# Optimization experiments

Hardware: AMD Instinct MI355X
Metric: run time of the kernel (lower is better)

## Reference

```python
import jax, jax.numpy as jnp
import numpy as np

N, K, IN, FEAT, H, OUT, E = 30000, 25, 64, 32, 128, 64, 480000


def setup_inputs() -> dict:
    key = jax.random.key(0)
    ks = jax.random.split(key, 24)
    w = lambda k, shp: (jax.random.normal(k, shp, dtype=jnp.float32) * 0.05)
    z = lambda n: jnp.zeros((n,), jnp.float32)
    return {
        "x": jax.random.normal(ks[0], (N, IN), jnp.float32),
        "dists_max": jax.random.uniform(ks[1], (N, K), jnp.float32),
        "dists_argmax": jax.random.randint(ks[2], (N, K), 0, N, jnp.int32),
        "edge_index": jax.random.randint(ks[3], (2, E), 0, N, jnp.int32),
        "train_mask": jnp.ones((E,), jnp.int32),
        # PGNN.linear_pre: in -> 32
        "w_pre": w(ks[4], (IN, FEAT)), "b_pre": z(FEAT),
        # conv_first (PGNN_layer(32, 128))
        "l1_dc_w1": w(ks[5], (1, H)), "l1_dc_b1": z(H),
        "l1_dc_w2": w(ks[6], (H, 1)), "l1_dc_b2": z(1),
        "l1_wh": w(ks[7], (2 * FEAT, H)), "l1_bh": z(H),
        "l1_wp": w(ks[8], (H, 1)), "l1_bp": z(1),
        # conv_out (PGNN_layer(128, 128))
        "l2_dc_w1": w(ks[9], (1, H)), "l2_dc_b1": z(H),
        "l2_dc_w2": w(ks[10], (H, 1)), "l2_dc_b2": z(1),
        "l2_wh": w(ks[11], (2 * H, H)), "l2_bh": z(H),
        "l2_wp": w(ks[12], (H, 1)), "l2_bp": z(1),
        # GNNModel.layers[1]: Linear(len_distmax=25 -> hidden=128)
        "w_lin": w(ks[13], (K, H)), "b_lin": z(H),
        # FeedForwardNetwork(2H -> 2H -> OUT)
        "ff_w1": w(ks[14], (2 * H, 2 * H)), "ff_b1": z(2 * H),
        "ff_w2": w(ks[15], (2 * H, OUT)), "ff_b2": z(OUT),
    }


def _nonlinear(d, w1, b1, w2, b2):
    # Nonlinear(1, H, 1) applied to dists: [N, K] -> [N, K]
    h = jax.nn.relu(d[..., None] @ w1 + b1)  # [N, K, H]
    return (h @ w2 + b2)[..., 0]


def _pgnn_layer(feat, dmax, argmax, dc_w1, dc_b1, dc_w2, dc_b2, wh, bh, wp, bp):
    d = _nonlinear(dmax, dc_w1, dc_b1, dc_w2, dc_b2)          # [N, K]
    sub = feat[argmax]                                         # gather: [N, K, F]
    self_feat = jnp.broadcast_to(feat[:, None, :], sub.shape)  # [N, K, F]
    msgs = jnp.concatenate([sub * d[..., None], self_feat], axis=-1)  # [N, K, 2F]
    msgs = jax.nn.relu(msgs @ wh + bh)                         # [N, K, H]
    out_position = (msgs @ wp + bp)[..., 0]                    # [N, K]
    out_structure = msgs.mean(axis=1)                          # [N, H]
    return out_position, out_structure


def reference(x, dists_max, dists_argmax, edge_index, train_mask,
              w_pre, b_pre,
              l1_dc_w1, l1_dc_b1, l1_dc_w2, l1_dc_b2, l1_wh, l1_bh, l1_wp, l1_bp,
              l2_dc_w1, l2_dc_b1, l2_dc_w2, l2_dc_b2, l2_wh, l2_bh, l2_wp, l2_bp,
              w_lin, b_lin, ff_w1, ff_b1, ff_w2, ff_b2):
    # PGNN (layer_num=2, feature_pre=True)
    h = x @ w_pre + b_pre                                      # [N, 32]
    _, h = _pgnn_layer(h, dists_max, dists_argmax,
                       l1_dc_w1, l1_dc_b1, l1_dc_w2, l1_dc_b2,
                       l1_wh, l1_bh, l1_wp, l1_bp)             # [N, H]
    x_pos, _ = _pgnn_layer(h, dists_max, dists_argmax,
                           l2_dc_w1, l2_dc_b1, l2_dc_w2, l2_dc_b2,
                           l2_wh, l2_bh, l2_wp, l2_bp)         # [N, K]
    # F.normalize(p=2, dim=-1) with eps=1e-12
    norm = jnp.maximum(jnp.linalg.norm(x_pos, axis=-1, keepdims=True), 1e-12)
    h = jax.nn.relu(x_pos / norm)                              # act after layer 0
    h = jax.nn.relu(h @ w_lin + b_lin)                         # layers[1] + act, [N, H]
    # get_minibatch_embeddings: select train edges, gather endpoint embeddings
    idx = np.where(np.asarray(train_mask) == 1)[0]
    ei = edge_index[:, idx]
    e = jnp.concatenate([h[ei[0]], h[ei[1]]], axis=1)          # [E_train, 2H]
    # FeedForwardNetwork
    e = jax.nn.relu(e @ ff_w1 + ff_b1)
    return e @ ff_w2 + ff_b2                                   # [E_train, OUT]
```

## Files before the change

kernel.cpp:

```cpp
#include <hip/hip_runtime.h>
#include <hip/hip_bf16.h>
#include <cmath>

#define NN 30000
#define KK 25
#define IN_F 64
#define FEAT 32
#define HH 128
#define OUTF 64
#define EE 480000
#define NPAGE 469
#define NB (8 * NPAGE)
#define LUTN 4096

typedef __attribute__((ext_vector_type(8))) _Float16 fp16x8;
typedef __attribute__((ext_vector_type(2))) _Float16 h2v;
typedef __attribute__((ext_vector_type(16))) float f32x16;

__device__ inline float u2f(unsigned u) { return __builtin_bit_cast(float, u); }
__device__ inline unsigned short f2b(float f) {
    __bf16 h = (__bf16)f;
    return __builtin_bit_cast(unsigned short, h);
}
__device__ inline unsigned short f2h(float f) {
    _Float16 h = (_Float16)f;
    return __builtin_bit_cast(unsigned short, h);
}
__device__ inline float blo(unsigned u) { return u2f(u << 16); }
__device__ inline float bhi(unsigned u) { return u2f(u & 0xffff0000u); }

__device__ inline unsigned hrelu2(unsigned a, unsigned b) {
    h2v x = __builtin_bit_cast(h2v, a);
    h2v y = __builtin_bit_cast(h2v, b);
    h2v s = x + y;
    h2v z = {(_Float16)0.f, (_Float16)0.f};
    h2v r = __builtin_elementwise_max(s, z);
    return __builtin_bit_cast(unsigned, r);
}

__device__ inline float lut_eval(const float* __restrict__ lut, float dm) {
    float tt = dm * (float)LUTN;
    int i0 = (int)tt;
    i0 = i0 < 0 ? 0 : (i0 > LUTN - 1 ? LUTN - 1 : i0);
    float f = tt - (float)i0;
    float l0 = lut[i0];
    return fmaf(lut[i0 + 1] - l0, f, l0);
}

__global__ void k_prep(const float* __restrict__ x,
                       const float* __restrict__ w_pre, const float* __restrict__ b_pre,
                       const float* __restrict__ l1wh, const float* __restrict__ l1bh,
                       const float* __restrict__ ffw2, const float* __restrict__ ffw1,
                       const float* __restrict__ l2wh,
                       const float* __restrict__ l1w1, const float* __restrict__ l1b1,
                       const float* __restrict__ l1w2, const float* __restrict__ l1b2,
                       const float* __restrict__ l2w1, const float* __restrict__ l2b1,
                       const float* __restrict__ l2w2, const float* __restrict__ l2b2,
                       unsigned* __restrict__ hist,
                       float* __restrict__ lut1, float* __restrict__ lut2,
                       unsigned short* __restrict__ xh, unsigned short* __restrict__ xl,
                       float* __restrict__ bfuse, unsigned short* __restrict__ wt,
                       unsigned short* __restrict__ wt1,
                       unsigned short* __restrict__ wt2h, unsigned short* __restrict__ wt2l,
                       unsigned short* __restrict__ wfh, unsigned short* __restrict__ wfl) {
    int gid = blockIdx.x * 256 + threadIdx.x;
    if (gid < NB) { hist[gid] = 0u; return; }
    gid -= NB;
    if (gid < 2 * (LUTN + 1)) {
        int which = gid / (LUTN + 1);
        int i = gid % (LUTN + 1);
        float dm = (float)i * (1.0f / (float)LUTN);
        const float* w1 = which ? l2w1 : l1w1;
        const float* b1 = which ? l2b1 : l1b1;
        const float* w2 = which ? l2w2 : l1w2;
        const float* b2 = which ? l2b2 : l1b2;
        float a = 0.f;
        for (int h = 0; h < HH; ++h)
            a = fmaf(fmaxf(fmaf(dm, w1[h], b1[h]), 0.f), w2[h], a);
        (which ? lut2 : lut1)[i] = a + b2[0];
        return;
    }
    gid -= 2 * (LUTN + 1);
    if (gid < NN * IN_F / 8) {
        int i = gid * 8;
        unsigned short vh[8], vl[8];
#pragma unroll
        for (int j = 0; j < 8; ++j) {
            float v = x[i + j];
            _Float16 hi = (_Float16)v;
            vh[j] = __builtin_bit_cast(unsigned short, hi);
            vl[j] = f2h((v - (float)hi) * 1024.f);
        }
        *(uint4*)(xh + i) = *(uint4*)vh;
        *(uint4*)(xl + i) = *(uint4*)vl;
        return;
    }
    gid -= NN * IN_F / 8;
    if (gid < 256) {
        int half = gid >> 7, h = gid & 127;
        const float* wh = l1wh + half * FEAT * HH + h;
        float acc = (half == 1) ? l1bh[h] : 0.f;
#pragma unroll
        for (int c = 0; c < FEAT; ++c) acc = fmaf(b_pre[c], wh[c * HH], acc);
        bfuse[gid] = acc;
    } else if (gid < 16640) {
        int i = gid - 256;
        int k = i >> 6, c = i & 63;
        wt[c * 256 + k] = f2h(ffw2[i]);
    } else if (gid < 82176) {
        int i = gid - 16640;
        int c = i >> 7, j = i & 127;
        float v = (c < 256) ? ffw1[j * 256 + c] : ffw1[(128 + j) * 256 + (c - 256)];
        wt1[c * 128 + j] = f2h(v);
    } else if (gid < 114944) {
        int i = gid - 82176;
        int c = i >> 7, j = i & 127;
        float v = (c < 128) ? l2wh[j * 128 + c] : l2wh[(128 + j) * 128 + (c - 128)];
        _Float16 hi = (_Float16)v;
        wt2h[c * 128 + j] = __builtin_bit_cast(unsigned short, hi);
        wt2l[c * 128 + j] = f2h((v - (float)hi) * 1024.f);
    } else if (gid < 131328) {
        int i = gid - 114944;
        int cc = i >> 6, j = i & 63;
        const float* wrow = w_pre + j * FEAT;
        float acc = 0.f;
#pragma unroll
        for (int c = 0; c < FEAT; ++c) {
            float wh = (cc < 128) ? l1wh[c * HH + cc] : l1wh[(FEAT + c) * HH + (cc - 128)];
            acc = fmaf(wrow[c], wh, acc);
        }
        _Float16 hi = (_Float16)acc;
        wfh[cc * 64 + j] = __builtin_bit_cast(unsigned short, hi);
        wfl[cc * 64 + j] = f2h((acc - (float)hi) * 1024.f);
    }
}

__global__ void k_hist(const int* __restrict__ ei, unsigned* __restrict__ hist) {
    int base = (blockIdx.x * 256 + threadIdx.x) * 8;
    if (base >= EE) return;
    int4 s0 = *(const int4*)(ei + base);
    int4 s1 = *(const int4*)(ei + base + 4);
    int4 d0 = *(const int4*)(ei + EE + base);
    int4 d1 = *(const int4*)(ei + EE + base + 4);
    int ss[8] = {s0.x, s0.y, s0.z, s0.w, s1.x, s1.y, s1.z, s1.w};
    int dd[8] = {d0.x, d0.y, d0.z, d0.w, d1.x, d1.y, d1.z, d1.w};
#pragma unroll
    for (int j = 0; j < 8; ++j) {
        int key = (ss[j] * 8 / NN) * NPAGE + (dd[j] >> 6);
        atomicAdd(&hist[key], 1u);
    }
}

__global__ __launch_bounds__(64) void k_scan(const unsigned* __restrict__ hist,
                                             unsigned* __restrict__ cursor) {
    int l = threadIdx.x;
    const int PER = 59;
    unsigned tot = 0;
    for (int j = 0; j < PER; ++j) {
        int i = l * PER + j;
        if (i < NB) tot += hist[i];
    }
    unsigned run = tot;
#pragma unroll
    for (int off = 1; off < 64; off <<= 1) {
        unsigned u = __shfl_up(run, off, 64);
        if (l >= off) run += u;
    }
    unsigned base = run - tot;
    for (int j = 0; j < PER; ++j) {
        int i = l * PER + j;
        if (i < NB) {
            cursor[i] = base;
            base += hist[i];
        }
    }
}

__global__ void k_scatter(const int* __restrict__ ei, unsigned* __restrict__ cursor,
                          uint4* __restrict__ sedge) {
    int base = (blockIdx.x * 256 + threadIdx.x) * 8;
    if (base >= EE) return;
    int4 s0 = *(const int4*)(ei + base);
    int4 s1 = *(const int4*)(ei + base + 4);
    int4 d0 = *(const int4*)(ei + EE + base);
    int4 d1 = *(const int4*)(ei + EE + base + 4);
    int ss[8] = {s0.x, s0.y, s0.z, s0.w, s1.x, s1.y, s1.z, s1.w};
    int dd[8] = {d0.x, d0.y, d0.z, d0.w, d1.x, d1.y, d1.z, d1.w};
    unsigned pp[8];
#pragma unroll
    for (int j = 0; j < 8; ++j) {
        int key = (ss[j] * 8 / NN) * NPAGE + (dd[j] >> 6);
        pp[j] = atomicAdd(&cursor[key], 1u);
    }
#pragma unroll
    for (int j = 0; j < 8; ++j)
        sedge[pp[j]] = make_uint4((unsigned)ss[j], (unsigned)dd[j], (unsigned)(base + j), 0u);
}

template <int KD>
__global__ __launch_bounds__(256) void k_nodegemm(
    const unsigned short* __restrict__ Ah, const unsigned short* __restrict__ Al,
    const unsigned short* __restrict__ Wh, const unsigned short* __restrict__ Wl,
    const float* __restrict__ gbias, const float* __restrict__ sbias,
    unsigned short* __restrict__ Gb, float* __restrict__ S) {
    int t = threadIdx.x;
    int l = t & 63, w = t >> 6;
    int c = l & 31, kh = l >> 5;
    int nb = blockIdx.x * 32;
    int na = nb + c;
    if (na >= NN) na = NN - 1;
    fp16x8 afh[KD / 16], afl[KD / 16];
#pragma unroll
    for (int kt = 0; kt < KD / 16; ++kt) {
        afh[kt] = *(const fp16x8*)(Ah + na * KD + kt * 16 + kh * 8);
        afl[kt] = *(const fp16x8*)(Al + na * KD + kt * 16 + kh * 8);
    }
    f32x16 acch0, acch1, accl0, accl1;
#pragma unroll
    for (int i = 0; i < 16; ++i) { acch0[i] = 0.f; acch1[i] = 0.f; accl0[i] = 0.f; accl1[i] = 0.f; }
    int cb0 = w * 64, cb1 = w * 64 + 32;
#pragma unroll
    for (int kt = 0; kt < KD / 16; ++kt) {
        fp16x8 b0h = *(const fp16x8*)(Wh + (cb0 + c) * KD + kt * 16 + kh * 8);
        fp16x8 b0l = *(const fp16x8*)(Wl + (cb0 + c) * KD + kt * 16 + kh * 8);
        fp16x8 b1h = *(const fp16x8*)(Wh + (cb1 + c) * KD + kt * 16 + kh * 8);
        fp16x8 b1l = *(const fp16x8*)(Wl + (cb1 + c) * KD + kt * 16 + kh * 8);
        acch0 = __builtin_amdgcn_mfma_f32_32x32x16_f16(afh[kt], b0h, acch0, 0, 0, 0);
        accl0 = __builtin_amdgcn_mfma_f32_32x32x16_f16(afh[kt], b0l, accl0, 0, 0, 0);
        accl0 = __builtin_amdgcn_mfma_f32_32x32x16_f16(afl[kt], b0h, accl0, 0, 0, 0);
        acch1 = __builtin_amdgcn_mfma_f32_32x32x16_f16(afh[kt], b1h, acch1, 0, 0, 0);
        accl1 = __builtin_amdgcn_mfma_f32_32x32x16_f16(afh[kt], b1l, accl1, 0, 0, 0);
        accl1 = __builtin_amdgcn_mfma_f32_32x32x16_f16(afl[kt], b1h, accl1, 0, 0, 0);
    }
    const float inv1024 = 1.0f / 1024.0f;
#pragma unroll
    for (int half = 0; half < 2; ++half) {
        int col = (half ? cb1 : cb0) + c;
        bool isG = col < HH;
        float gb_ = (isG && gbias) ? gbias[col] : 0.f;
        float sb_ = (!isG) ? sbias[col - HH] : 0.f;
#pragma unroll
        for (int r = 0; r < 16; ++r) {
            int row = (r & 3) + 8 * (r >> 2) + 4 * kh;
            int n = nb + row;
            float v = half ? (acch1[r] + accl1[r] * inv1024)
                           : (acch0[r] + accl0[r] * inv1024);
            if (n < NN) {
                if (isG) Gb[n * HH + col] = f2b(v + gb_);
                else S[n * HH + (col - HH)] = v + sb_;
            }
        }
    }
}

__global__ void k_layer1(const unsigned* __restrict__ G1u, const float* __restrict__ S1,
                         const float* __restrict__ dmax, const float* __restrict__ lut1,
                         const int* __restrict__ amax,
                         unsigned* __restrict__ hh, unsigned* __restrict__ hl) {
    int t = threadIdx.x;
    int n = blockIdx.x * 4 + (t >> 6);
    int l = t & 63;
    float2 sv = *(const float2*)(S1 + n * HH + 2 * l);
    const int* arow = amax + n * KK;
    const float* drow = dmax + n * KK;
    float dk[KK];
#pragma unroll
    for (int k = 0; k < KK; ++k) dk[k] = lut_eval(lut1, drow[k]);
    float acc0 = 0.f, acc1 = 0.f;
#pragma unroll
    for (int k = 0; k < KK; ++k) {
        int a = arow[k];
        unsigned g = G1u[a * 64 + l];
        acc0 += fmaxf(fmaf(dk[k], blo(g), sv.x), 0.f);
        acc1 += fmaxf(fmaf(dk[k], bhi(g), sv.y), 0.f);
    }
    float a0 = acc0 * 0.04f, a1 = acc1 * 0.04f;
    _Float16 h0 = (_Float16)a0, h1v = (_Float16)a1;
    float r0 = (a0 - (float)h0) * 1024.f, r1 = (a1 - (float)h1v) * 1024.f;
    hh[n * 64 + l] = (unsigned)__builtin_bit_cast(unsigned short, h0) |
                     ((unsigned)__builtin_bit_cast(unsigned short, h1v) << 16);
    hl[n * 64 + l] = (unsigned)f2h(r0) | ((unsigned)f2h(r1) << 16);
}

__global__ __launch_bounds__(256) void k_xpos2(
    const unsigned* __restrict__ G2u, const float* __restrict__ S2,
    const float* __restrict__ dmax, const float* __restrict__ lut2,
    const int* __restrict__ amax,
    const float* __restrict__ wp, const float* __restrict__ bp,
    const float* __restrict__ wlin, const float* __restrict__ blin,
    unsigned short* __restrict__ hl16) {
    __shared__ float xs[28];
    int t = threadIdx.x;
    int n = blockIdx.x;
    int w = t >> 6, l = t & 63;
    float2 sv = *(const float2*)(S2 + n * HH + 2 * l);
    float2 wpv = *(const float2*)(wp + 2 * l);
    float bpv = bp[0];
    const int* arow = amax + n * KK;
    const float* drow = dmax + n * KK;
    int kcnt = (w == 0) ? 7 : 6;
    unsigned gv[7];
    float dk[7];
#pragma unroll
    for (int j = 0; j < 7; ++j) {
        if (j < kcnt) {
            int k = w + 4 * j;
            gv[j] = G2u[arow[k] * 64 + l];
        }
    }
#pragma unroll
    for (int j = 0; j < 7; ++j) {
        if (j < kcnt) dk[j] = lut_eval(lut2, drow[w + 4 * j]);
    }
    float v[7];
#pragma unroll
    for (int j = 0; j < 7; ++j) {
        if (j < kcnt) {
            v[j] = fmaxf(fmaf(dk[j], blo(gv[j]), sv.x), 0.f) * wpv.x +
                   fmaxf(fmaf(dk[j], bhi(gv[j]), sv.y), 0.f) * wpv.y;
        }
    }
#pragma unroll
    for (int s = 1; s < 64; s <<= 1) {
#pragma unroll
        for (int j = 0; j < 7; ++j) {
            if (j < kcnt) v[j] += __shfl_xor(v[j], s, 64);
        }
    }
    if (l == 0) {
#pragma unroll
        for (int j = 0; j < 7; ++j) {
            if (j < kcnt) xs[w + 4 * j] = v[j] + bpv;
        }
    }
    __syncthreads();
    if (t < HH) {
        float ss = 0.f;
#pragma unroll
        for (int k = 0; k < KK; ++k) { float xv = xs[k]; ss = fmaf(xv, xv, ss); }
        float inv = 1.0f / fmaxf(sqrtf(ss), 1e-12f);
        float acc = blin[t];
#pragma unroll
        for (int k = 0; k < KK; ++k) {
            float xv = fmaxf(xs[k], 0.f) * inv;
            acc = fmaf(xv, wlin[k * HH + t], acc);
        }
        hl16[n * HH + t] = f2h(fmaxf(acc, 0.f));
    }
}

__global__ __launch_bounds__(256) void k_ab_mfma(
    const unsigned short* __restrict__ hl16, const unsigned short* __restrict__ wt1,
    const float* __restrict__ ffb1, unsigned short* __restrict__ ab) {
    int t = threadIdx.x;
    int l = t & 63, w = t >> 6;
    int c = l & 31, kh = l >> 5;
    int nb = blockIdx.x * 32;
    int na = nb + c;
    if (na >= NN) na = NN - 1;
    fp16x8 af[8];
#pragma unroll
    for (int kt = 0; kt < 8; ++kt)
        af[kt] = *(const fp16x8*)(hl16 + na * 128 + kt * 16 + kh * 8);
    f32x16 acc[4];
#pragma unroll
    for (int g = 0; g < 4; ++g)
#pragma unroll
        for (int i = 0; i < 16; ++i) acc[g][i] = 0.f;
#pragma unroll
    for (int kt = 0; kt < 8; ++kt) {
#pragma unroll
        for (int g = 0; g < 4; ++g) {
            fp16x8 b = *(const fp16x8*)(wt1 + (w * 128 + g * 32 + c) * 128 + kt * 16 + kh * 8);
            acc[g] = __builtin_amdgcn_mfma_f32_32x32x16_f16(af[kt], b, acc[g], 0, 0, 0);
        }
    }
#pragma unroll
    for (int g = 0; g < 4; ++g) {
        int col = w * 128 + g * 32 + c;
        float bias = (col >= 256) ? ffb1[col - 256] : 0.f;
#pragma unroll
        for (int r = 0; r < 16; ++r) {
            int row = (r & 3) + 8 * (r >> 2) + 4 * kh;
            int n = nb + row;
            if (n < NN) ab[n * 512 + col] = f2h(acc[g][r] + bias);
        }
    }
}

__global__ __launch_bounds__(256, 2) void k_edge_mfma(
    const unsigned short* __restrict__ abf, const uint4* __restrict__ sedge,
    const unsigned short* __restrict__ wt, const float* __restrict__ ffb2,
    float* __restrict__ out) {
    __shared__ uint4 P[4][32 * 32];
    int t = threadIdx.x;
    int l = t & 63;
    int w = t >> 6;
    int c = l & 31, kh = l >> 5;
    uint4* Pw = P[w];

    fp16x8 wf0[16], wf1[16];
#pragma unroll
    for (int kt = 0; kt < 16; ++kt) {
        wf0[kt] = *(const fp16x8*)(wt + c * 256 + kt * 16 + kh * 8);
        wf1[kt] = *(const fp16x8*)(wt + (c + 32) * 256 + kt * 16 + kh * 8);
    }
    float bias0 = ffb2[c], bias1 = ffb2[c + 32];

    int xcd = blockIdx.x & 7;
    int slot = blockIdx.x >> 3;
    int seg = c;
    int rh = l >> 5;

    for (int tl = slot; tl < NPAGE; tl += 64) {
        int tbw = (xcd * NPAGE + tl) * 128 + w * 32;
#pragma unroll 4
        for (int it = 0; it < 16; ++it) {
            int row = it * 2 + rh;
            int pos = tbw + row;
            uint4 rec = sedge[pos < EE ? pos : EE - 1];
            uint4 a = *(const uint4*)(abf + (size_t)rec.x * 512 + seg * 8);
            uint4 b = *(const uint4*)(abf + (size_t)rec.y * 512 + 256 + seg * 8);
            uint4 p;
            p.x = hrelu2(a.x, b.x);
            p.y = hrelu2(a.y, b.y);
            p.z = hrelu2(a.z, b.z);
            p.w = hrelu2(a.w, b.w);
            Pw[row * 32 + (seg ^ (row & 15))] = p;
        }
        asm volatile("s_waitcnt lgkmcnt(0)" ::: "memory");
        __builtin_amdgcn_sched_barrier(0);
        f32x16 acc0, acc1;
#pragma unroll
        for (int i = 0; i < 16; ++i) { acc0[i] = 0.f; acc1[i] = 0.f; }
#pragma unroll
        for (int kt = 0; kt < 16; ++kt) {
            int idx = (kt * 2 + kh) ^ (c & 15);
            fp16x8 af = __builtin_bit_cast(fp16x8, Pw[c * 32 + idx]);
            acc0 = __builtin_amdgcn_mfma_f32_32x32x16_f16(af, wf0[kt], acc0, 0, 0, 0);
            acc1 = __builtin_amdgcn_mfma_f32_32x32x16_f16(af, wf1[kt], acc1, 0, 0, 0);
        }
        int spos = tbw + c;
        int eid = (int)sedge[spos < EE ? spos : EE - 1].z;
        int rbase = 4 * kh;
#pragma unroll
        for (int r = 0; r < 16; ++r) {
            int row = (r & 3) + 8 * (r >> 2) + rbase;
            int eidr = __shfl(eid, row, 64);
            if (tbw + row < EE) {
                size_t o = (size_t)eidr * 64;
                out[o + c] = acc0[r] + bias0;
                out[o + 32 + c] = acc1[r] + bias1;
            }
        }
        __builtin_amdgcn_sched_barrier(0);
    }
}

extern "C" void kernel_launch(void* const* d_in, const int* in_sizes, int n_in,
                              void* d_out, int out_size, void* d_ws, size_t ws_size,
                              hipStream_t stream) {
    const float* x     = (const float*)d_in[0];
    const float* dmax  = (const float*)d_in[1];
    const int*   amax  = (const int*)d_in[2];
    const int*   ei    = (const int*)d_in[3];
    const float* w_pre = (const float*)d_in[5];
    const float* b_pre = (const float*)d_in[6];
    const float* l1w1  = (const float*)d_in[7];
    const float* l1b1  = (const float*)d_in[8];
    const float* l1w2  = (const float*)d_in[9];
    const float* l1b2  = (const float*)d_in[10];
    const float* l1wh  = (const float*)d_in[11];
    const float* l1bh  = (const float*)d_in[12];
    const float* l2w1  = (const float*)d_in[15];
    const float* l2b1  = (const float*)d_in[16];
    const float* l2w2  = (const float*)d_in[17];
    const float* l2b2  = (const float*)d_in[18];
    const float* l2wh  = (const float*)d_in[19];
    const float* l2bh  = (const float*)d_in[20];
    const float* l2wp  = (const float*)d_in[21];
    const float* l2bp  = (const float*)d_in[22];
    const float* wlin  = (const float*)d_in[23];
    const float* blin  = (const float*)d_in[24];
    const float* ffw1  = (const float*)d_in[25];
    const float* ffb1  = (const float*)d_in[26];
    const float* ffw2  = (const float*)d_in[27];
    const float* ffb2  = (const float*)d_in[28];

    float* ws = (float*)d_ws;
    unsigned short* Gb = (unsigned short*)(ws + 1500000);
    float* S  = ws + 3500000;
    unsigned short* xh = (unsigned short*)(ws + 7500000);
    unsigned short* xl = (unsigned short*)(ws + 8500000);
    unsigned* hhp = (unsigned*)(ws + 9500000);
    unsigned* hlp = (unsigned*)(ws + 11500000);
    unsigned short* hl16 = (unsigned short*)(ws + 13500000);
    uint4* sedge = (uint4*)(ws + 15500000);
    unsigned short* wfh = (unsigned short*)(ws + 17500000);
    unsigned short* wfl = (unsigned short*)(ws + 17510000);
    float* bfuse = ws + 17520000;
    unsigned short* wt = (unsigned short*)(ws + 17530000);
    unsigned short* wt1 = (unsigned short*)(ws + 17540000);
    unsigned short* wt2h = (unsigned short*)(ws + 17580000);
    unsigned short* wt2l = (unsigned short*)(ws + 17600000);
    unsigned* hist = (unsigned*)(ws + 17620000);
    unsigned* cursor = (unsigned*)(ws + 17630000);
    float* lut1 = ws + 17640000;
    float* lut2 = ws + 17645000;
    unsigned short* ab = (unsigned short*)ws;
    float* out = (float*)d_out;

    k_prep<<<1498, 256, 0, stream>>>(x, w_pre, b_pre, l1wh, l1bh, ffw2, ffw1, l2wh,
                                     l1w1, l1b1, l1w2, l1b2, l2w1, l2b1, l2w2, l2b2,
                                     hist, lut1, lut2, xh, xl,
                                     bfuse, wt, wt1, wt2h, wt2l, wfh, wfl);
    k_hist<<<(EE / 8 + 255) / 256, 256, 0, stream>>>(ei, hist);
    k_scan<<<1, 64, 0, stream>>>(hist, cursor);
    k_scatter<<<(EE / 8 + 255) / 256, 256, 0, stream>>>(ei, cursor, sedge);

    k_nodegemm<IN_F><<<938, 256, 0, stream>>>(xh, xl, wfh, wfl, bfuse, bfuse + 128, Gb, S);
    k_layer1<<<NN / 4, 256, 0, stream>>>((const unsigned*)Gb, S, dmax, lut1, amax, hhp, hlp);
    k_nodegemm<HH><<<938, 256, 0, stream>>>((const unsigned short*)hhp,
                                            (const unsigned short*)hlp, wt2h, wt2l,
                                            nullptr, l2bh, Gb, S);
    k_xpos2<<<NN, 256, 0, stream>>>((const unsigned*)Gb, S, dmax, lut2, amax,
                                    l2wp, l2bp, wlin, blin, hl16);
    k_ab_mfma<<<938, 256, 0, stream>>>(hl16, wt1, ffb1, ab);

    k_edge_mfma<<<512, 256, 0, stream>>>(ab, sedge, wt, ffb2, out);
}
```

Measured before the change: 364.1 us.

## Restructure xpos2 to one node per wave and share edge tile block-wide

k_layer1 and k_xpos2 now issue all 25 gathers up front, ahead of the LUT evaluation, so more loads are in flight at once. k_xpos2 is remapped so each wave handles a whole node: it reduces all 25 positions with shuffles, does the normalize and the 25-to-128 linear layer in registers, and drops the shared-memory pass and block barrier. The grid shrinks fourfold. k_edge_mfma now builds one shared 128-row tile cooperatively with all 256 threads and uses __syncthreads instead of per-wave LDS regions, at the cost of block-level synchronisation and higher register pressure from the 25-entry arrays.

```diff
diff --git a/kernel.cpp b/kernel.cpp
--- a/kernel.cpp
+++ b/kernel.cpp
@@ -263,16 +263,18 @@
     float2 sv = *(const float2*)(S1 + n * HH + 2 * l);
     const int* arow = amax + n * KK;
     const float* drow = dmax + n * KK;
-    float dk[KK];
-#pragma unroll
-    for (int k = 0; k < KK; ++k) dk[k] = lut_eval(lut1, drow[k]);
+    unsigned gvv[KK];
+#pragma unroll
+    for (int k = 0; k < KK; ++k) gvv[k] = G1u[arow[k] * 64 + l];
+    float dm_[KK];
+#pragma unroll
+    for (int k = 0; k < KK; ++k) dm_[k] = drow[k];
     float acc0 = 0.f, acc1 = 0.f;
 #pragma unroll
     for (int k = 0; k < KK; ++k) {
-        int a = arow[k];
-        unsigned g = G1u[a * 64 + l];
-        acc0 += fmaxf(fmaf(dk[k], blo(g), sv.x), 0.f);
-        acc1 += fmaxf(fmaf(dk[k], bhi(g), sv.y), 0.f);
+        float dkv = lut_eval(lut1, dm_[k]);
+        acc0 += fmaxf(fmaf(dkv, blo(gvv[k]), sv.x), 0.f);
+        acc1 += fmaxf(fmaf(dkv, bhi(gvv[k]), sv.y), 0.f);
     }
     float a0 = acc0 * 0.04f, a1 = acc1 * 0.04f;
     _Float16 h0 = (_Float16)a0, h1v = (_Float16)a1;
@@ -288,65 +290,47 @@
     const int* __restrict__ amax,
     const float* __restrict__ wp, const float* __restrict__ bp,
     const float* __restrict__ wlin, const float* __restrict__ blin,
-    unsigned short* __restrict__ hl16) {
-    __shared__ float xs[28];
+    unsigned* __restrict__ hl16u) {
     int t = threadIdx.x;
-    int n = blockIdx.x;
     int w = t >> 6, l = t & 63;
+    int n = blockIdx.x * 4 + w;
     float2 sv = *(const float2*)(S2 + n * HH + 2 * l);
     float2 wpv = *(const float2*)(wp + 2 * l);
-    float bpv = bp[0];
     const int* arow = amax + n * KK;
     const float* drow = dmax + n * KK;
-    int kcnt = (w == 0) ? 7 : 6;
-    unsigned gv[7];
-    float dk[7];
-#pragma unroll
-    for (int j = 0; j < 7; ++j) {
-        if (j < kcnt) {
-            int k = w + 4 * j;
-            gv[j] = G2u[arow[k] * 64 + l];
-        }
-    }
-#pragma unroll
-    for (int j = 0; j < 7; ++j) {
-        if (j < kcnt) dk[j] = lut_eval(lut2, drow[w + 4 * j]);
-    }
-    float v[7];
-#pragma unroll
-    for (int j = 0; j < 7; ++j) {
-        if (j < kcnt) {
-            v[j] = fmaxf(fmaf(dk[j], blo(gv[j]), sv.x), 0.f) * wpv.x +
-                   fmaxf(fmaf(dk[j], bhi(gv[j]), sv.y), 0.f) * wpv.y;
-        }
+    unsigned gvv[KK];
+#pragma unroll
+    for (int k = 0; k < KK; ++k) gvv[k] = G2u[arow[k] * 64 + l];
+    float dm_[KK];
+#pragma unroll
+    for (int k = 0; k < KK; ++k) dm_[k] = drow[k];
+    float v[KK];
+#pragma unroll
+    for (int k = 0; k < KK; ++k) {
+        float dkv = lut_eval(lut2, dm_[k]);
+        v[k] = fmaxf(fmaf(dkv, blo(gvv[k]), sv.x), 0.f) * wpv.x +
+               fmaxf(fmaf(dkv, bhi(gvv[k]), sv.y), 0.f) * wpv.y;
     }
 #pragma unroll
     for (int s = 1; s < 64; s <<= 1) {
 #pragma unroll
-        for (int j = 0; j < 7; ++j) {
-            if (j < kcnt) v[j] += __shfl_xor(v[j], s, 64);
-        }
-    }
-    if (l == 0) {
-#pragma unroll
-        for (int j = 0; j < 7; ++j) {
-            if (j < kcnt) xs[w + 4 * j] = v[j] + bpv;
-        }
-    }
-    __syncthreads();
-    if (t < HH) {
-        float ss = 0.f;
-#pragma unroll
-        for (int k = 0; k < KK; ++k) { float xv = xs[k]; ss = fmaf(xv, xv, ss); }
-        float inv = 1.0f / fmaxf(sqrtf(ss), 1e-12f);
-        float acc = blin[t];
-#pragma unroll
-        for (int k = 0; k < KK; ++k) {
-            float xv = fmaxf(xs[k], 0.f) * inv;
-            acc = fmaf(xv, wlin[k * HH + t], acc);
-        }
-        hl16[n * HH + t] = f2h(fmaxf(acc, 0.f));
-    }
+        for (int k = 0; k < KK; ++k) v[k] += __shfl_xor(v[k], s, 64);
+    }
+    float bpv = bp[0];
+    float ss = 0.f;
+#pragma unroll
+    for (int k = 0; k < KK; ++k) { v[k] += bpv; ss = fmaf(v[k], v[k], ss); }
+    float inv = 1.0f / fmaxf(sqrtf(ss), 1e-12f);
+    float acc0 = blin[2 * l], acc1 = blin[2 * l + 1];
+#pragma unroll
+    for (int k = 0; k < KK; ++k) {
+        float xv = fmaxf(v[k], 0.f) * inv;
+        float2 wl = *(const float2*)(wlin + k * HH + 2 * l);
+        acc0 = fmaf(xv, wl.x, acc0);
+        acc1 = fmaf(xv, wl.y, acc1);
+    }
+    hl16u[n * 64 + l] = (unsigned)f2h(fmaxf(acc0, 0.f)) |
+                        ((unsigned)f2h(fmaxf(acc1, 0.f)) << 16);
 }
 
 __global__ __launch_bounds__(256) void k_ab_mfma(
@@ -392,12 +376,11 @@
     const unsigned short* __restrict__ abf, const uint4* __restrict__ sedge,
     const unsigned short* __restrict__ wt, const float* __restrict__ ffb2,
     float* __restrict__ out) {
-    __shared__ uint4 P[4][32 * 32];
+    __shared__ uint4 P[128 * 32];
     int t = threadIdx.x;
     int l = t & 63;
     int w = t >> 6;
     int c = l & 31, kh = l >> 5;
-    uint4* Pw = P[w];
 
     fp16x8 wf0[16], wf1[16];
 #pragma unroll
@@ -409,15 +392,15 @@
 
     int xcd = blockIdx.x & 7;
     int slot = blockIdx.x >> 3;
-    int seg = c;
-    int rh = l >> 5;
+    int seg = t & 31;
+    int rb = t >> 5;
 
     for (int tl = slot; tl < NPAGE; tl += 64) {
-        int tbw = (xcd * NPAGE + tl) * 128 + w * 32;
+        int tb = (xcd * NPAGE + tl) * 128;
 #pragma unroll 4
-        for (int it = 0; it < 16; ++it) {
-            int row = it * 2 + rh;
-            int pos = tbw + row;
+        for (int r = 0; r < 16; ++r) {
+            int row = r * 8 + rb;
+            int pos = tb + row;
             uint4 rec = sedge[pos < EE ? pos : EE - 1];
             uint4 a = *(const uint4*)(abf + (size_t)rec.x * 512 + seg * 8);
             uint4 b = *(const uint4*)(abf + (size_t)rec.y * 512 + 256 + seg * 8);
@@ -426,34 +409,36 @@
             p.y = hrelu2(a.y, b.y);
             p.z = hrelu2(a.z, b.z);
             p.w = hrelu2(a.w, b.w);
-            Pw[row * 32 + (seg ^ (row & 15))] = p;
-        }
-        asm volatile("s_waitcnt lgkmcnt(0)" ::: "memory");
-        __builtin_amdgcn_sched_barrier(0);
+            int col = (seg * 16) ^ ((row & 15) << 4);
+            P[row * 32 + (col >> 4)] = p;
+        }
+        __syncthreads();
         f32x16 acc0, acc1;
 #pragma unroll
         for (int i = 0; i < 16; ++i) { acc0[i] = 0.f; acc1[i] = 0.f; }
+        int wrow = w * 32 + c;
+        int sw = (wrow & 15) << 4;
 #pragma unroll
         for (int kt = 0; kt < 16; ++kt) {
-            int idx = (kt * 2 + kh) ^ (c & 15);
-            fp16x8 af = __builtin_bit_cast(fp16x8, Pw[c * 32 + idx]);
+            int col = (kt * 32 + kh * 16) ^ sw;
+            fp16x8 af = __builtin_bit_cast(fp16x8, P[wrow * 32 + (col >> 4)]);
             acc0 = __builtin_amdgcn_mfma_f32_32x32x16_f16(af, wf0[kt], acc0, 0, 0, 0);
             acc1 = __builtin_amdgcn_mfma_f32_32x32x16_f16(af, wf1[kt], acc1, 0, 0, 0);
         }
-        int spos = tbw + c;
+        int spos = tb + wrow;
         int eid = (int)sedge[spos < EE ? spos : EE - 1].z;
         int rbase = 4 * kh;
 #pragma unroll
         for (int r = 0; r < 16; ++r) {
             int row = (r & 3) + 8 * (r >> 2) + rbase;
             int eidr = __shfl(eid, row, 64);
-            if (tbw + row < EE) {
+            if (tb + w * 32 + row < EE) {
                 size_t o = (size_t)eidr * 64;
                 out[o + c] = acc0[r] + bias0;
                 out[o + 32 + c] = acc1[r] + bias1;
             }
         }
-        __builtin_amdgcn_sched_barrier(0);
+        __syncthreads();
     }
 }
 
@@ -523,8 +508,8 @@
     k_nodegemm<HH><<<938, 256, 0, stream>>>((const unsigned short*)hhp,
                                             (const unsigned short*)hlp, wt2h, wt2l,
                                             nullptr, l2bh, Gb, S);
-    k_xpos2<<<NN, 256, 0, stream>>>((const unsigned*)Gb, S, dmax, lut2, amax,
-                                    l2wp, l2bp, wlin, blin, hl16);
+    k_xpos2<<<NN / 4, 256, 0, stream>>>((const unsigned*)Gb, S, dmax, lut2, amax,
+                                        l2wp, l2bp, wlin, blin, (unsigned*)hl16);
     k_ab_mfma<<<938, 256, 0, stream>>>(hl16, wt1, ffb1, ab);
 
     k_edge_mfma<<<512, 256, 0, stream>>>(ab, sedge, wt, ffb2, out);
```

New measurement: 367.3 us. Within noise of the previous version (+0.9%).
